# Optimization experiments

Hardware: AMD Instinct MI355X
Metric: run time of the kernel (lower is better)

## Reference

```python
import jax, jax.numpy as jnp
import numpy as np

B, N, M, U, L = 2048, 256, 128, 512, 2   # batch, memory locations, memory width, num_units, num_layers
RH, WH, SH = 2, 2, 1                      # read heads, write heads, conv_shift_range
CLIP = 20.0
HEAD_R = M + 3 + (2 * SH + 1)             # 134 = k(M)+beta+g+s(2r+1)+gamma
HEAD_W = HEAD_R + 2 * M                   # 390 = + erase(M) + add(M)


def setup_inputs():
    key = jax.random.key(0)
    ks = jax.random.split(key, 12)
    def nrm(k, shape, s=0.05):
        return jax.random.normal(k, shape, jnp.float32) * s
    return {
        "X": jax.random.normal(ks[0], (B, U), jnp.float32),
        "m0": nrm(ks[1], (1, N, M), 0.5),
        "H0": nrm(ks[2], (L, 1, U)),
        "C0": nrm(ks[3], (L, 1, U)),
        "R0": nrm(ks[4], (RH, 1, M)),
        "A0": nrm(ks[5], (RH + WH, 1, N)),
        "W_prep": nrm(ks[6], (M * RH, U)),
        "b_prep": jnp.zeros((U,), jnp.float32),
        "W_lstm": nrm(ks[7], (L, 3 * U, 4 * U)),
        "b_lstm": jnp.zeros((L, 4 * U), jnp.float32),
        "W_r": nrm(ks[8], (U, RH * HEAD_R)),
        "b_r": jnp.zeros((RH * HEAD_R,), jnp.float32),
        "W_w": nrm(ks[9], (U, WH * HEAD_W)),
        "b_w": jnp.zeros((WH * HEAD_W,), jnp.float32),
        "W_ou": nrm(ks[10], (U + RH * M, U)),
        "b_ou": jnp.zeros((U,), jnp.float32),
    }


def _addressing(k, beta, g, s, gamma, m, a_prev):
    # k [B,M], beta/g/gamma [B], s [B,2*SH+1], m [B,N,M], a_prev [B,N]
    inner = jnp.einsum('bnm,bm->bn', m, k)
    k_norm = jnp.sqrt(jnp.sum(k * k, axis=1, keepdims=True))   # [B,1]
    m_norm = jnp.sqrt(jnp.sum(m * m, axis=2))                  # [B,N]
    K = inner / (k_norm * m_norm + 1e-8)
    w_c = jax.nn.softmax(beta[:, None] * K, axis=1)            # exp/sum in source == softmax
    w_g = g[:, None] * w_c + (1.0 - g[:, None]) * a_prev
    # The stacked-slice s_matrix in the source is exactly circular convolution:
    # w_conv[i] = sum_d s_d * w_g[(i - d) mod N], d in {0..SH, -SH..-1} matching s layout.
    shifts = list(range(0, SH + 1)) + list(range(-SH, 0))
    w_conv = sum(s[:, j:j + 1] * jnp.roll(w_g, shifts[j], axis=1) for j in range(2 * SH + 1))
    w_sharp = w_conv ** gamma[:, None]
    return w_sharp / jnp.sum(w_sharp, axis=1, keepdims=True)


def reference(X, m0, H0, C0, R0, A0, W_prep, b_prep, W_lstm, b_lstm,
              W_r, b_r, W_w, b_w, W_ou, b_ou):
    b = X.shape[0]
    m = jnp.broadcast_to(m0, (b, N, M))
    R_prev = [jnp.broadcast_to(jnp.tanh(R0[i]), (b, M)) for i in range(RH)]
    A_prev = [jnp.broadcast_to(jax.nn.softmax(A0[i], axis=-1), (b, N)) for i in range(RH + WH)]

    # controller
    h = jnp.concatenate(R_prev, axis=1) @ W_prep + b_prep
    for l in range(L):
        x_in = jnp.concatenate([X, h], axis=1)                              # [B,2U]
        h_prev = jnp.broadcast_to(H0[l], (b, U))
        c_prev = jnp.broadcast_to(C0[l], (b, U))
        z = jnp.concatenate([x_in, h_prev], axis=1) @ W_lstm[l] + b_lstm[l]  # [B,4U]
        i_g, f_g, g_g, o_g = jnp.split(z, 4, axis=1)
        c = jax.nn.sigmoid(f_g) * c_prev + jax.nn.sigmoid(i_g) * jnp.tanh(g_g)
        h = jax.nn.sigmoid(o_g) * jnp.tanh(c)
    h = jnp.clip(h, -CLIP, CLIP)

    r_heads = (h @ W_r + b_r).reshape(b, RH, HEAD_R)
    w_heads = (h @ W_w + b_w).reshape(b, WH, HEAD_W)
    heads = [r_heads[:, i] for i in range(RH)] + [w_heads[:, i] for i in range(WH)]

    A_t = []
    for ii, hd in enumerate(heads):
        A_t.append(_addressing(
            k=jnp.tanh(hd[:, :M]),
            beta=jax.nn.softplus(hd[:, M]),
            g=jax.nn.sigmoid(hd[:, M + 1]),
            s=jax.nn.softmax(hd[:, M + 2:M + 2 + 2 * SH + 1], axis=-1),
            gamma=jax.nn.softplus(hd[:, M + 2 + 2 * SH + 1]),
            m=m, a_prev=A_prev[ii]))

    # reads from old memory
    R_t = [jnp.einsum('bn,bnm->bm', A_t[i], m) for i in range(RH)]

    # sequential erase/add writes
    m_t = m
    for ii in range(WH):
        w = A_t[RH + ii][:, :, None]                                  # [B,N,1]
        del_v = jax.nn.sigmoid(w_heads[:, ii, -2 * M:-M])[:, None, :]  # [B,1,M]
        add_v = jnp.tanh(w_heads[:, ii, -M:])[:, None, :]
        m_t = m_t * (1.0 - w * del_v) + w * add_v

    y = jnp.clip(jnp.concatenate([h] + R_t, axis=1) @ W_ou + b_ou, -CLIP, CLIP)
    return y, m_t
```

## Files before the change

### kernel.cpp

```cpp
#include <hip/hip_runtime.h>
#include <math.h>

static constexpr int Bn = 2048;
static constexpr int Nn = 256;
static constexpr int Mn = 128;
static constexpr int Un = 512;

static constexpr size_t OFF_MNORM = 4608;
static constexpr size_t OFF_APREV = 4864;
static constexpr size_t OFF_BIASH = 5888;
static constexpr size_t OFF_KMAT  = 16384;
static constexpr size_t OFF_HEADS = OFF_KMAT + (size_t)8192 * 256;
static constexpr size_t OFF_AT    = OFF_HEADS + (size_t)2048 * 1048;
static constexpr size_t OFF_ERA   = OFF_AT + (size_t)2 * 2048 * 256;
static constexpr size_t OFF_ADD   = OFF_ERA + (size_t)2048 * 256;
static constexpr size_t OFF_XHB   = OFF_ADD + (size_t)2048 * 256;
static constexpr size_t OFF_HCAT  = OFF_XHB + 524288;
static constexpr size_t OFF_W0T   = OFF_HCAT + 524288;
static constexpr size_t OFF_W1T   = OFF_W0T + 524288;
static constexpr size_t OFF_WRWT  = OFF_W1T + 1048576;
static constexpr size_t OFF_WCOMB = OFF_WRWT + 294912;
static constexpr size_t OFF_WR2T  = OFF_WCOMB + 262144;
static constexpr size_t OFF_M0B   = OFF_WR2T + 65536;
static constexpr size_t OFF_ZPART = OFF_M0B + 16384 + 524288;

static constexpr int S_X0  = 0;
static constexpr int S_M0  = 512;
static constexpr int S_W0  = 528;
static constexpr int S_W1  = 1552;
static constexpr int S_WR  = 3600;
static constexpr int S_WW  = 3744;
static constexpr int S_WOU = 4144;
static constexpr int S_WR2 = 4400;
static constexpr int S_CA  = 4528;
static constexpr int S_ZC  = 4529;
static constexpr int S_END = 4657;

#define DEV __device__ __forceinline__

typedef __attribute__((ext_vector_type(8))) short bf16x8;
typedef __attribute__((ext_vector_type(4))) float f32x4;
typedef __attribute__((ext_vector_type(8))) unsigned short ushort8;
typedef unsigned int u32;

DEV float sigf(float x) { return 1.0f / (1.0f + expf(-x)); }
DEV float softplusf(float x) { return x > 20.0f ? x : log1pf(expf(x)); }
DEV unsigned short f2bf(float f) {
    unsigned u = __float_as_uint(f);
    u = (u + 0x7FFFu + ((u >> 16) & 1u)) >> 16;
    return (unsigned short)u;
}
DEV void gload16(const unsigned short* g, unsigned short* l) {
    __builtin_amdgcn_global_load_lds(
        (const __attribute__((address_space(1))) u32*)g,
        (__attribute__((address_space(3))) u32*)l, 16, 0, 0);
}

DEV float blk_reduce_max(float v, float* red) {
    int tid = threadIdx.x;
    red[tid] = v; __syncthreads();
    for (int s = (int)blockDim.x >> 1; s > 0; s >>= 1) {
        if (tid < s) red[tid] = fmaxf(red[tid], red[tid + s]);
        __syncthreads();
    }
    float r = red[0]; __syncthreads();
    return r;
}
DEV float blk_reduce_sum(float v, float* red) {
    int tid = threadIdx.x;
    red[tid] = v; __syncthreads();
    for (int s = (int)blockDim.x >> 1; s > 0; s >>= 1) {
        if (tid < s) red[tid] += red[tid + s];
        __syncthreads();
    }
    float r = red[0]; __syncthreads();
    return r;
}

DEV float wv_sum(float v) {
    #pragma unroll
    for (int off = 32; off; off >>= 1) v += __shfl_xor(v, off);
    return v;
}
DEV float wv_max(float v) {
    #pragma unroll
    for (int off = 32; off; off >>= 1) v = fmaxf(v, __shfl_xor(v, off));
    return v;
}
DEV float blk_sum4(float v, float* red4) {
    v = wv_sum(v);
    int w = threadIdx.x >> 6;
    if ((threadIdx.x & 63) == 0) red4[w] = v;
    __syncthreads();
    float r = red4[0] + red4[1] + red4[2] + red4[3];
    __syncthreads();
    return r;
}
DEV float blk_max4(float v, float* red4) {
    v = wv_max(v);
    int w = threadIdx.x >> 6;
    if ((threadIdx.x & 63) == 0) red4[w] = v;
    __syncthreads();
    float r = fmaxf(fmaxf(red4[0], red4[1]), fmaxf(red4[2], red4[3]));
    __syncthreads();
    return r;
}

#define GEMM_STAGE(buf, k0)                                                     \
    {                                                                           \
        _Pragma("unroll")                                                       \
        for (int q = 0; q < 2; ++q)                                             \
            gload16(A  + (size_t)(row0 + q * 32 + (tid >> 3)) * lda + (k0) + ke,\
                    &As[buf][q * 2048 + tid * 8]);                              \
        _Pragma("unroll")                                                       \
        for (int q = 0; q < 4; ++q)                                             \
            gload16(Wt + (size_t)(col0 + q * 32 + (tid >> 3)) * ldw + (k0) + ke,\
                    &Ws[buf][q * 2048 + tid * 8]);                              \
    }

#define GEMM_PROLOG_CORE                                                        \
    __shared__ __align__(16) unsigned short As[2][64 * 64];                     \
    __shared__ __align__(16) unsigned short Ws[2][128 * 64];                    \
    const int tid  = threadIdx.x;                                               \
    const int lane = tid & 63;                                                  \
    const int wave = tid >> 6;                                                  \
    const int wr = wave >> 1, wc = wave & 1;                                    \
    const int ke = ((tid & 7) * 8) ^ (((tid >> 3) & 7) << 3);                   \
    const int frow = lane & 15;                                                 \
    const int fko  = (lane >> 4) * 8;                                           \
    const int fxm  = (frow & 7) << 3;                                           \
    f32x4 acc[2][4];                                                            \
    _Pragma("unroll")                                                           \
    for (int i = 0; i < 2; ++i)                                                 \
        _Pragma("unroll")                                                       \
        for (int j = 0; j < 4; ++j) acc[i][j] = (f32x4){0.f, 0.f, 0.f, 0.f};

#define GEMM_PROLOG                                                             \
    GEMM_PROLOG_CORE                                                            \
    const int row0 = blockIdx.x * 64;                                           \
    const int col0 = blockIdx.y * 128;

#define GEMM_FRAGS_AND_MFMA(Ab, Wb)                                             \
    {                                                                           \
        bf16x8 af[2][2], wf[2][4];                                              \
        _Pragma("unroll")                                                       \
        for (int kk = 0; kk < 2; ++kk) {                                        \
            _Pragma("unroll")                                                   \
            for (int i = 0; i < 2; ++i) {                                       \
                int fr = wr * 32 + i * 16 + frow;                               \
                af[kk][i] = *(const bf16x8*)&(Ab)[fr * 64 + ((kk * 32 + fko) ^ fxm)]; \
            }                                                                   \
            _Pragma("unroll")                                                   \
            for (int j = 0; j < 4; ++j) {                                       \
                int fr = wc * 64 + j * 16 + frow;                               \
                wf[kk][j] = *(const bf16x8*)&(Wb)[fr * 64 + ((kk * 32 + fko) ^ fxm)]; \
            }                                                                   \
        }                                                                       \
        __builtin_amdgcn_s_setprio(1);                                          \
        _Pragma("unroll")                                                       \
        for (int kk = 0; kk < 2; ++kk)                                          \
            _Pragma("unroll")                                                   \
            for (int i = 0; i < 2; ++i)                                         \
                _Pragma("unroll")                                               \
                for (int j = 0; j < 4; ++j)                                     \
                    acc[i][j] = __builtin_amdgcn_mfma_f32_16x16x32_bf16(        \
                        af[kk][i], wf[kk][j], acc[i][j], 0, 0, 0);              \
        __builtin_amdgcn_s_setprio(0);                                          \
    }

#define GEMM_MAINLOOP(Kr)                                                       \
    {                                                                           \
        const int nt = (Kr) >> 6;                                               \
        int cur = 0;                                                            \
        GEMM_STAGE(0, 0);                                                       \
        for (int t = 0; t < nt; ++t) {                                          \
            if (t + 1 < nt) {                                                   \
                GEMM_STAGE(cur ^ 1, (t + 1) * 64);                              \
                asm volatile("s_waitcnt vmcnt(6)" ::: "memory");                \
            } else {                                                            \
                asm volatile("s_waitcnt vmcnt(0)" ::: "memory");                \
            }                                                                   \
            __builtin_amdgcn_sched_barrier(0);                                  \
            __builtin_amdgcn_s_barrier();                                       \
            __builtin_amdgcn_sched_barrier(0);                                  \
            GEMM_FRAGS_AND_MFMA(As[cur], Ws[cur]);                              \
            __builtin_amdgcn_sched_barrier(0);                                  \
            __builtin_amdgcn_s_barrier();                                       \
            cur ^= 1;                                                           \
        }                                                                       \
    }

__global__ __launch_bounds__(256) void gemm_bf16(
    const unsigned short* __restrict__ A, int lda,
    const unsigned short* __restrict__ Wt, int ldw,
    const float* __restrict__ bias,
    float* __restrict__ C, unsigned short* __restrict__ Cb, int ldc,
    int Nr, int Kr, int epi)
{
    GEMM_PROLOG
    GEMM_MAINLOOP(Kr)
    #pragma unroll
    for (int i = 0; i < 2; ++i) {
        int m0r = row0 + wr * 32 + i * 16 + (lane >> 4) * 4;
        #pragma unroll
        for (int j = 0; j < 4; ++j) {
            int n = col0 + wc * 64 + j * 16 + (lane & 15);
            if (n >= Nr) continue;
            float bv = bias ? bias[n] : 0.f;
            #pragma unroll
            for (int r = 0; r < 4; ++r) {
                float v = acc[i][j][r] + bv;
                if (epi == 1) v = fminf(fmaxf(v, -20.f), 20.f);
                if (epi == 2) Cb[(size_t)(m0r + r) * ldc + n] = f2bf(v);
                else          C [(size_t)(m0r + r) * ldc + n] = v;
            }
        }
    }
}

__global__ __launch_bounds__(256) void gemm_lstm(
    const unsigned short* __restrict__ A, int lda,
    const unsigned short* __restrict__ Wt, int ldw,
    const float* __restrict__ zpart, const float* __restrict__ b_lstm,
    int z, const float* __restrict__ c0,
    unsigned short* __restrict__ hout, int ldh, int Kr, int doclip)
{
    GEMM_PROLOG
    GEMM_MAINLOOP(Kr)
    const int uu = lane & 15;
    const int q  = (col0 >> 6) + wc;
    const int uq = q * 16 + uu;
    const float c0v = c0[uq];
    float bg[4];
    #pragma unroll
    for (int g = 0; g < 4; ++g) {
        int j = g * 512 + q * 16 + uu;
        float a = b_lstm[z * 2048 + j];
        #pragma unroll
        for (int p = 0; p < 8; ++p)
            a += zpart[((size_t)z * 8 + p) * 2048 + j];
        bg[g] = a;
    }
    #pragma unroll
    for (int i = 0; i < 2; ++i) {
        int rbase = row0 + wr * 32 + i * 16 + (lane >> 4) * 4;
        #pragma unroll
        for (int r = 0; r < 4; ++r) {
            float ig = acc[i][0][r] + bg[0];
            float fg = acc[i][1][r] + bg[1];
            float gg = acc[i][2][r] + bg[2];
            float og = acc[i][3][r] + bg[3];
            float c = sigf(fg) * c0v + sigf(ig) * tanhf(gg);
            float h = sigf(og) * tanhf(c);
            if (doclip) h = fminf(fmaxf(h, -20.f), 20.f);
            hout[(size_t)(rbase + r) * ldh + uq] = f2bf(h);
        }
    }
}

__global__ __launch_bounds__(256) void gemm_l0p(
    const unsigned short* __restrict__ XHB,
    const unsigned short* __restrict__ W0T,
    const unsigned short* __restrict__ WR2T,
    const unsigned short* __restrict__ M0B,
    const float* __restrict__ zpart, const float* __restrict__ b_lstm,
    const float* __restrict__ c0, unsigned short* __restrict__ hout,
    unsigned short* __restrict__ WCOMB)
{
    const int by = blockIdx.y, bx = blockIdx.x;
    const unsigned short *A, *Wt;
    int lda, ldw, row0, col0, Kr;
    unsigned short* pCb = nullptr;
    if (by < 16) {
        A = XHB;  lda = 1024; Wt = W0T; ldw = 512;
        row0 = bx * 64; col0 = by * 128; Kr = 512;
    } else {
        int pz = bx >> 4, py = (bx >> 3) & 1, px = bx & 7;
        A = WR2T + pz * 128; lda = 256; Wt = M0B; ldw = 128;
        row0 = px * 64; col0 = py * 128; Kr = 128;
        pCb = WCOMB + 512 + pz * 256;
    }
    GEMM_PROLOG_CORE
    GEMM_MAINLOOP(Kr)
    if (by < 16) {
        const int uu = lane & 15;
        const int q  = (col0 >> 6) + wc;
        const int uq = q * 16 + uu;
        const float c0v = c0[uq];
        float bg[4];
        #pragma unroll
        for (int g = 0; g < 4; ++g) {
            int j = g * 512 + q * 16 + uu;
            float a = b_lstm[j];
            #pragma unroll
            for (int p = 0; p < 8; ++p)
                a += zpart[(size_t)p * 2048 + j];
            bg[g] = a;
        }
        #pragma unroll
        for (int i = 0; i < 2; ++i) {
            int rbase = row0 + wr * 32 + i * 16 + (lane >> 4) * 4;
            #pragma unroll
            for (int r = 0; r < 4; ++r) {
                float ig = acc[i][0][r] + bg[0];
                float fg = acc[i][1][r] + bg[1];
                float gg = acc[i][2][r] + bg[2];
                float og = acc[i][3][r] + bg[3];
                float c = sigf(fg) * c0v + sigf(ig) * tanhf(gg);
                float h = sigf(og) * tanhf(c);
                hout[(size_t)(rbase + r) * 1024 + uq] = f2bf(h);
            }
        }
    } else {
        #pragma unroll
        for (int i = 0; i < 2; ++i) {
            int m0r = row0 + wr * 32 + i * 16 + (lane >> 4) * 4;
            #pragma unroll
            for (int j = 0; j < 4; ++j) {
                int n = col0 + wc * 64 + j * 16 + (lane & 15);
                #pragma unroll
                for (int r = 0; r < 4; ++r)
                    pCb[(size_t)(m0r + r) * 1024 + n] = f2bf(acc[i][j][r]);
            }
        }
    }
}

__global__ __launch_bounds__(256) void gemm_kmat(
    const float* __restrict__ heads,
    const unsigned short* __restrict__ M0B,
    float* __restrict__ C)
{
    GEMM_PROLOG_CORE
    const int row0 = blockIdx.x * 64;
    const int col0 = blockIdx.y * 128;

#define KMAT_STAGE(buf, k0)                                                     \
    {                                                                           \
        _Pragma("unroll")                                                       \
        for (int q = 0; q < 2; ++q) {                                           \
            int R = row0 + q * 32 + (tid >> 3);                                 \
            int b = R >> 2, ih = R & 3;                                         \
            int cb = (ih < 2) ? ih * 134 : 268 + (ih - 2) * 390;                \
            const float* hp = heads + (size_t)b * 1048 + cb + (k0) + ke;        \
            ushort8 o;                                                          \
            _Pragma("unroll")                                                   \
            for (int j = 0; j < 8; ++j) o[j] = f2bf(tanhf(hp[j]));              \
            *(ushort8*)&As[buf][q * 2048 + tid * 8] = o;                        \
        }                                                                       \
        _Pragma("unroll")                                                       \
        for (int q = 0; q < 4; ++q)                                             \
            gload16(M0B + (size_t)(col0 + q * 32 + (tid >> 3)) * 128 + (k0) + ke,\
                    &Ws[buf][q * 2048 + tid * 8]);                              \
    }

    int cur = 0;
    KMAT_STAGE(0, 0);
    for (int t = 0; t < 2; ++t) {
        __syncthreads();
        if (t == 0) KMAT_STAGE(1, 64);
        GEMM_FRAGS_AND_MFMA(As[cur], Ws[cur]);
        cur ^= 1;
    }
#undef KMAT_STAGE
    #pragma unroll
    for (int i = 0; i < 2; ++i) {
        int m0r = row0 + wr * 32 + i * 16 + (lane >> 4) * 4;
        #pragma unroll
        for (int j = 0; j < 4; ++j) {
            int n = col0 + wc * 64 + j * 16 + (lane & 15);
            #pragma unroll
            for (int r = 0; r < 4; ++r)
                C[(size_t)(m0r + r) * 256 + n] = acc[i][j][r];
        }
    }
}

DEV void dev_cvt8(const float* src, int lds, unsigned short* dst, int ldd,
                  int c8, int bloc, int tid)
{
    size_t idx = (size_t)bloc * 256 + tid;
    size_t r = idx / c8, c = (idx % c8) * 8;
    const float* s = src + r * lds + c;
    float4 v0 = *(const float4*)s;
    float4 v1 = *(const float4*)(s + 4);
    ushort8 o;
    o[0] = f2bf(v0.x); o[1] = f2bf(v0.y); o[2] = f2bf(v0.z); o[3] = f2bf(v0.w);
    o[4] = f2bf(v1.x); o[5] = f2bf(v1.y); o[6] = f2bf(v1.z); o[7] = f2bf(v1.w);
    *(ushort8*)(dst + r * ldd + c) = o;
}

DEV void dev_cvtT(const float* src, int R, int C, int lds,
                  unsigned short* dst, int ldd, int mode, int bx, int by,
                  int tid, float* t )
{
    const int x = tid & 31;
    for (int y = tid >> 5; y < 32; y += 8) {
        int r = by * 32 + y, c = bx * 32 + x;
        int scol = c;
        if (mode) scol = ((c >> 4) & 3) * 512 + (c >> 6) * 16 + (c & 15);
        t[y * 33 + x] = (r < R && c < C) ? src[(size_t)r * lds + scol] : 0.f;
    }
    __syncthreads();
    for (int y = tid >> 5; y < 32; y += 8) {
        int c = bx * 32 + y, r = by * 32 + x;
        if (c < C && r < R) dst[(size_t)c * ldd + r] = f2bf(t[x * 33 + y]);
    }
}

__global__ __launch_bounds__(256) void k_prep(
    const float* __restrict__ X, const float* __restrict__ m0,
    const float* __restrict__ H0, const float* __restrict__ R0,
    const float* __restrict__ A0, const float* __restrict__ W_prep,
    const float* __restrict__ b_prep, const float* __restrict__ W_lstm,
    const float* __restrict__ W_r, const float* __restrict__ b_r,
    const float* __restrict__ W_w, const float* __restrict__ b_w,
    const float* __restrict__ W_ou, float* __restrict__ ws)
{
    __shared__ float sh[32 * 33 + 64];
    const int bid = blockIdx.x, tid = threadIdx.x;
    unsigned short* XHB   = (unsigned short*)(ws + OFF_XHB);
    unsigned short* W0T   = (unsigned short*)(ws + OFF_W0T);
    unsigned short* W1T   = (unsigned short*)(ws + OFF_W1T);
    unsigned short* WRWT  = (unsigned short*)(ws + OFF_WRWT);
    unsigned short* WCOMB = (unsigned short*)(ws + OFF_WCOMB);
    unsigned short* WR2T  = (unsigned short*)(ws + OFF_WR2T);
    unsigned short* M0B   = (unsigned short*)(ws + OFF_M0B);

    if (bid < S_M0) {
        dev_cvt8(X, 512, XHB, 1024, 64, bid - S_X0, tid);
    } else if (bid < S_W0) {
        dev_cvt8(m0, 128, M0B, 128, 16, bid - S_M0, tid);
    } else if (bid < S_W1) {
        int s = bid - S_W0;
        dev_cvtT(W_lstm, 512, 2048, 2048, W0T, 512, 1, s & 63, s >> 6, tid, sh);
    } else if (bid < S_WR) {
        int s = bid - S_W1;
        dev_cvtT(W_lstm + (size_t)1536 * 2048, 1024, 2048, 2048, W1T, 1024, 1,
                 s & 63, s >> 6, tid, sh);
    } else if (bid < S_WW) {
        int s = bid - S_WR;
        dev_cvtT(W_r, 512, 268, 268, WRWT, 512, 0, s % 9, s / 9, tid, sh);
    } else if (bid < S_WOU) {
        int s = bid - S_WW;
        dev_cvtT(W_w, 512, 780, 780, WRWT + (size_t)268 * 512, 512, 0,
                 s % 25, s / 25, tid, sh);
    } else if (bid < S_WR2) {
        int s = bid - S_WOU;
        dev_cvtT(W_ou, 512, 512, 512, WCOMB, 1024, 0, s & 15, s >> 4, tid, sh);
    } else if (bid < S_CA) {
        int s = bid - S_WR2;
        dev_cvtT(W_ou + (size_t)512 * 512, 256, 512, 512, WR2T, 256, 0,
                 s & 15, s >> 4, tid, sh);
    } else if (bid < S_ZC) {
        float* red = sh;
        for (int i = 0; i < 4; ++i) {
            float v = A0[i * 256 + tid];
            float mx = blk_reduce_max(v, red);
            float e = expf(v - mx);
            float s = blk_reduce_sum(e, red);
            ws[OFF_APREV + i * 256 + tid] = e / s;
        }
        float acc = 0.f;
        for (int m = 0; m < 128; ++m) {
            float t = m0[(size_t)tid * 128 + m];
            acc = fmaf(t, t, acc);
        }
        ws[OFF_MNORM + tid] = sqrtf(acc);
        for (int j = tid; j < 1152; j += 256)
            ws[OFF_BIASH + j] = (j < 268) ? b_r[j] : (j < 1048 ? b_w[j - 268] : 0.f);
    } else {
        int sub = bid - S_ZC;
        int colb = sub & 7, up = (sub >> 3) & 7, z = sub >> 6;
        int j = colb * 256 + tid;
        float acc = 0.f;
        if (z == 0) {
            if (up < 4) {
                sh[256 + tid] = tanhf(R0[tid]);
                __syncthreads();
                if (tid < 128) {
                    int u = up * 128 + tid;
                    float a = b_prep[u];
                    for (int k = 0; k < 256; ++k)
                        a = fmaf(sh[256 + k], W_prep[(size_t)k * 512 + u], a);
                    sh[tid] = a;
                }
                __syncthreads();
                const int u0 = up * 128;
                #pragma unroll 4
                for (int t = 0; t < 128; ++t)
                    acc = fmaf(sh[t], W_lstm[(size_t)(512 + u0 + t) * 2048 + j], acc);
            } else {
                const int u0 = up * 128;
                #pragma unroll 4
                for (int t = 0; t < 128; ++t)
                    acc = fmaf(H0[u0 - 512 + t],
                               W_lstm[(size_t)(512 + u0 + t) * 2048 + j], acc);
            }
        } else {
            const int u0 = up * 64;
            const float* W1 = W_lstm + (size_t)1536 * 2048;
            #pragma unroll 4
            for (int t = 0; t < 64; ++t)
                acc = fmaf(H0[512 + u0 + t], W1[(size_t)(1024 + u0 + t) * 2048 + j], acc);
        }
        (ws + OFF_ZPART)[((size_t)z * 8 + up) * 2048 + j] = acc;
    }
}

__global__ __launch_bounds__(256) void k_addr(
    const float* __restrict__ heads, const float* __restrict__ kmat,
    const float* __restrict__ mnorm, const float* __restrict__ aprev,
    float* __restrict__ at, unsigned short* __restrict__ hcat,
    float* __restrict__ era, float* __restrict__ addv)
{
    __shared__ float red4[4];
    __shared__ float wgs[256];
    __shared__ float sc[6];
    const int b = blockIdx.x, i = blockIdx.y, tid = threadIdx.x;
    const int cb = (i < 2) ? i * 134 : 268 + (i - 2) * 390;
    const float* hd = heads + (size_t)b * 1048 + cb;
    float kv = (tid < 128) ? tanhf(hd[tid]) : 0.f;
    float kn = sqrtf(blk_sum4(kv * kv, red4));
    if (i >= 2 && tid < 128) {
        era [((size_t)b * 2 + (i - 2)) * 128 + tid] = sigf(hd[134 + tid]);
        addv[((size_t)b * 2 + (i - 2)) * 128 + tid] = tanhf(hd[262 + tid]);
    }
    if (tid == 0) {
        sc[0] = softplusf(hd[128]);
        sc[1] = sigf(hd[129]);
        float v0 = hd[130], v1 = hd[131], v2 = hd[132];
        float mx = fmaxf(v0, fmaxf(v1, v2));
        float e0 = expf(v0 - mx), e1 = expf(v1 - mx), e2 = expf(v2 - mx);
        float ssum = e0 + e1 + e2;
        sc[2] = e0 / ssum; sc[3] = e1 / ssum; sc[4] = e2 / ssum;
        sc[5] = softplusf(hd[133]);
    }
    __syncthreads();
    const float beta = sc[0], g = sc[1], s0 = sc[2], s1 = sc[3], s2 = sc[4],
                gamma = sc[5];
    float inner = kmat[((size_t)b * 4 + i) * 256 + tid];
    float K = inner / (kn * mnorm[tid] + 1e-8f);
    float x = beta * K;
    float mx = blk_max4(x, red4);
    float e = expf(x - mx);
    float se = blk_sum4(e, red4);
    float wc = e / se;
    float wg = g * wc + (1.f - g) * aprev[i * 256 + tid];
    wgs[tid] = wg;
    __syncthreads();
    float wconv = s0 * wg + s1 * wgs[(tid + 255) & 255] + s2 * wgs[(tid + 1) & 255];
    float wsh = powf(wconv, gamma);
    float ssum = blk_sum4(wsh, red4);
    float w = wsh / ssum;
    if (i < 2) hcat[(size_t)b * 1024 + 512 + i * 256 + tid] = f2bf(w);
    else       at[((size_t)(i - 2) * Bn + b) * 256 + tid] = w;
}

__global__ __launch_bounds__(512) void k_memt(
    const float* __restrict__ m0, const float* __restrict__ at,
    const float* __restrict__ era, const float* __restrict__ addv,
    float* __restrict__ outm)
{
    __shared__ __align__(16) float at_s[2][8][256];
    __shared__ __align__(16) float er_s[2][8][128];
    __shared__ __align__(16) float ad_s[2][8][128];
    const int tid = threadIdx.x;
    const int b0 = blockIdx.x * 8;
    for (int t = tid; t < 1024; t += 512) {
        int i = t >> 9, rem = t & 511;
        int bb = rem >> 6, n4 = rem & 63;
        ((float4*)&at_s[i][bb][0])[n4] =
            ((const float4*)(at + ((size_t)i * Bn + b0 + bb) * 256))[n4];
    }
    {
        int t = tid;
        if (t < 512) {
            int i = t >> 8, rem = t & 255;
            int bb = rem >> 5, m4 = rem & 31;
            ((float4*)&er_s[i][bb][0])[m4] =
                ((const float4*)(era + ((size_t)(b0 + bb) * 2 + i) * 128))[m4];
            ((float4*)&ad_s[i][bb][0])[m4] =
                ((const float4*)(addv + ((size_t)(b0 + bb) * 2 + i) * 128))[m4];
        }
    }
    __syncthreads();
    const float4* m0v = (const float4*)m0;
    float4* outv = (float4*)outm;
    for (int pos = tid; pos < 8192; pos += 512) {
        int mq = pos & 31, n = pos >> 5;
        float4 t0 = m0v[pos];
        #pragma unroll
        for (int bb = 0; bb < 8; ++bb) {
            float w0 = at_s[0][bb][n], w1 = at_s[1][bb][n];
            float4 e0 = *(const float4*)&er_s[0][bb][mq * 4];
            float4 a0 = *(const float4*)&ad_s[0][bb][mq * 4];
            float4 e1 = *(const float4*)&er_s[1][bb][mq * 4];
            float4 a1 = *(const float4*)&ad_s[1][bb][mq * 4];
            float4 t = t0;
#define UPD(c) { t.c = t.c * (1.f - w0 * e0.c) + w0 * a0.c; \
                 t.c = t.c * (1.f - w1 * e1.c) + w1 * a1.c; }
            UPD(x) UPD(y) UPD(z) UPD(w)
#undef UPD
            __builtin_nontemporal_store(*(f32x4*)&t,
                (f32x4*)&outv[(size_t)(b0 + bb) * 8192 + pos]);
        }
    }
}

extern "C" void kernel_launch(void* const* d_in, const int* in_sizes, int n_in,
                              void* d_out, int out_size, void* d_ws, size_t ws_size,
                              hipStream_t stream)
{
    const float* X      = (const float*)d_in[0];
    const float* m0     = (const float*)d_in[1];
    const float* H0     = (const float*)d_in[2];
    const float* C0     = (const float*)d_in[3];
    const float* R0     = (const float*)d_in[4];
    const float* A0     = (const float*)d_in[5];
    const float* W_prep = (const float*)d_in[6];
    const float* b_prep = (const float*)d_in[7];
    const float* W_lstm = (const float*)d_in[8];
    const float* b_lstm = (const float*)d_in[9];
    const float* W_r    = (const float*)d_in[10];
    const float* b_r    = (const float*)d_in[11];
    const float* W_w    = (const float*)d_in[12];
    const float* b_w    = (const float*)d_in[13];
    const float* W_ou   = (const float*)d_in[14];
    const float* b_ou   = (const float*)d_in[15];
    float* ws  = (float*)d_ws;
    float* out = (float*)d_out;

    unsigned short* XHB   = (unsigned short*)(ws + OFF_XHB);
    unsigned short* HCAT  = (unsigned short*)(ws + OFF_HCAT);
    unsigned short* W0T   = (unsigned short*)(ws + OFF_W0T);
    unsigned short* W1T   = (unsigned short*)(ws + OFF_W1T);
    unsigned short* WRWT  = (unsigned short*)(ws + OFF_WRWT);
    unsigned short* WCOMB = (unsigned short*)(ws + OFF_WCOMB);
    unsigned short* WR2T  = (unsigned short*)(ws + OFF_WR2T);
    unsigned short* M0B   = (unsigned short*)(ws + OFF_M0B);

    k_prep<<<S_END, 256, 0, stream>>>(
        X, m0, H0, R0, A0, W_prep, b_prep, W_lstm, W_r, b_r, W_w, b_w, W_ou, ws);

    gemm_l0p<<<dim3(32, 17), 256, 0, stream>>>(
        XHB, W0T, WR2T, M0B, ws + OFF_ZPART, b_lstm, C0, XHB + 512, WCOMB);

    gemm_lstm<<<dim3(32, 16), 256, 0, stream>>>(
        XHB, 1024, W1T, 1024, ws + OFF_ZPART, b_lstm, 1, C0 + 512, HCAT, 1024, 1024, 1);

    gemm_bf16<<<dim3(32, 9), 256, 0, stream>>>(
        HCAT, 1024, WRWT, 512, ws + OFF_BIASH, ws + OFF_HEADS, nullptr, 1048, 1048, 512, 0);

    gemm_kmat<<<dim3(128, 2), 256, 0, stream>>>(
        ws + OFF_HEADS, M0B, ws + OFF_KMAT);

    k_addr<<<dim3(Bn, 4), 256, 0, stream>>>(
        ws + OFF_HEADS, ws + OFF_KMAT, ws + OFF_MNORM, ws + OFF_APREV,
        ws + OFF_AT, HCAT, ws + OFF_ERA, ws + OFF_ADD);

    gemm_bf16<<<dim3(32, 4), 256, 0, stream>>>(
        HCAT, 1024, WCOMB, 1024, b_ou, out, nullptr, 512, 512, 1024, 1);

    k_memt<<<256, 512, 0, stream>>>(
        m0, ws + OFF_AT, ws + OFF_ERA, ws + OFF_ADD, out + (size_t)Bn * Un);
}
```

Measured before the change: 185.3 us.

## Re-partition weight prep across kernels and merge output GEMM with memory write

```diff
diff --git a/kernel.cpp b/kernel.cpp
--- a/kernel.cpp
+++ b/kernel.cpp
@@ -24,17 +24,26 @@
 static constexpr size_t OFF_M0B   = OFF_WR2T + 65536;
 static constexpr size_t OFF_ZPART = OFF_M0B + 16384 + 524288;
 
-static constexpr int S_X0  = 0;
-static constexpr int S_M0  = 512;
-static constexpr int S_W0  = 528;
-static constexpr int S_W1  = 1552;
-static constexpr int S_WR  = 3600;
-static constexpr int S_WW  = 3744;
-static constexpr int S_WOU = 4144;
-static constexpr int S_WR2 = 4400;
-static constexpr int S_CA  = 4528;
-static constexpr int S_ZC  = 4529;
-static constexpr int S_END = 4657;
+static constexpr int P_X0  = 0;
+static constexpr int P_M0  = 512;
+static constexpr int P_W0  = 528;
+static constexpr int P_WR2 = 1552;
+static constexpr int P_CA  = 1680;
+static constexpr int P_ZC  = 1681;
+static constexpr int P_END = 1745;
+
+static constexpr int M_L0  = 0;
+static constexpr int M_PF  = 512;
+static constexpr int M_W1  = 544;
+static constexpr int M_WRr = 2592;
+static constexpr int M_WRw = 2736;
+static constexpr int M_WOU = 3136;
+static constexpr int M_ZC1 = 3392;
+static constexpr int M_END = 3456;
+
+static constexpr int T_OUT = 0;
+static constexpr int T_MEM = 128;
+static constexpr int T_END = 384;
 
 #define DEV __device__ __forceinline__
 
@@ -106,21 +115,11 @@
     return r;
 }
 
-#define GEMM_STAGE(buf, k0)                                                     \
-    {                                                                           \
-        _Pragma("unroll")                                                       \
-        for (int q = 0; q < 2; ++q)                                             \
-            gload16(A  + (size_t)(row0 + q * 32 + (tid >> 3)) * lda + (k0) + ke,\
-                    &As[buf][q * 2048 + tid * 8]);                              \
-        _Pragma("unroll")                                                       \
-        for (int q = 0; q < 4; ++q)                                             \
-            gload16(Wt + (size_t)(col0 + q * 32 + (tid >> 3)) * ldw + (k0) + ke,\
-                    &Ws[buf][q * 2048 + tid * 8]);                              \
-    }
-
-#define GEMM_PROLOG_CORE                                                        \
+#define GEMM_SHARED                                                             \
     __shared__ __align__(16) unsigned short As[2][64 * 64];                     \
-    __shared__ __align__(16) unsigned short Ws[2][128 * 64];                    \
+    __shared__ __align__(16) unsigned short Ws[2][128 * 64];
+
+#define GEMM_REGS                                                               \
     const int tid  = threadIdx.x;                                               \
     const int lane = tid & 63;                                                  \
     const int wave = tid >> 6;                                                  \
@@ -135,10 +134,17 @@
         _Pragma("unroll")                                                       \
         for (int j = 0; j < 4; ++j) acc[i][j] = (f32x4){0.f, 0.f, 0.f, 0.f};
 
-#define GEMM_PROLOG                                                             \
-    GEMM_PROLOG_CORE                                                            \
-    const int row0 = blockIdx.x * 64;                                           \
-    const int col0 = blockIdx.y * 128;
+#define GEMM_STAGE(buf, k0)                                                     \
+    {                                                                           \
+        _Pragma("unroll")                                                       \
+        for (int q = 0; q < 2; ++q)                                             \
+            gload16(A  + (size_t)(row0 + q * 32 + (tid >> 3)) * lda + (k0) + ke,\
+                    &As[buf][q * 2048 + tid * 8]);                              \
+        _Pragma("unroll")                                                       \
+        for (int q = 0; q < 4; ++q)                                             \
+            gload16(Wt + (size_t)(col0 + q * 32 + (tid >> 3)) * ldw + (k0) + ke,\
+                    &Ws[buf][q * 2048 + tid * 8]);                              \
+    }
 
 #define GEMM_FRAGS_AND_MFMA(Ab, Wb)                                             \
     {                                                                           \
@@ -190,14 +196,249 @@
         }                                                                       \
     }
 
+#define LSTM_EPILOGUE(zc, doclip, houtp, ldhv)                                  \
+    {                                                                           \
+        const int uu = lane & 15;                                               \
+        const int q  = (col0 >> 6) + wc;                                        \
+        const int uq = q * 16 + uu;                                             \
+        const float c0v = c0[(zc) * 512 + uq];                                  \
+        float bg[4];                                                            \
+        _Pragma("unroll")                                                       \
+        for (int g = 0; g < 4; ++g) {                                           \
+            int j = g * 512 + q * 16 + uu;                                      \
+            float a = b_lstm[(zc) * 2048 + j];                                  \
+            _Pragma("unroll")                                                   \
+            for (int p = 0; p < 8; ++p)                                         \
+                a += zpart[((size_t)(zc) * 8 + p) * 2048 + j];                  \
+            bg[g] = a;                                                          \
+        }                                                                       \
+        _Pragma("unroll")                                                       \
+        for (int i = 0; i < 2; ++i) {                                           \
+            int rbase = row0 + wr * 32 + i * 16 + (lane >> 4) * 4;              \
+            _Pragma("unroll")                                                   \
+            for (int r = 0; r < 4; ++r) {                                       \
+                float ig = acc[i][0][r] + bg[0];                                \
+                float fg = acc[i][1][r] + bg[1];                                \
+                float gg = acc[i][2][r] + bg[2];                                \
+                float og = acc[i][3][r] + bg[3];                                \
+                float c = sigf(fg) * c0v + sigf(ig) * tanhf(gg);                \
+                float h = sigf(og) * tanhf(c);                                  \
+                if (doclip) h = fminf(fmaxf(h, -20.f), 20.f);                   \
+                (houtp)[(size_t)(rbase + r) * (ldhv) + uq] = f2bf(h);           \
+            }                                                                   \
+        }                                                                       \
+    }
+
+DEV void dev_cvt8(const float* src, int lds, unsigned short* dst, int ldd,
+                  int c8, int bloc, int tid)
+{
+    size_t idx = (size_t)bloc * 256 + tid;
+    size_t r = idx / c8, c = (idx % c8) * 8;
+    const float* s = src + r * lds + c;
+    float4 v0 = *(const float4*)s;
+    float4 v1 = *(const float4*)(s + 4);
+    ushort8 o;
+    o[0] = f2bf(v0.x); o[1] = f2bf(v0.y); o[2] = f2bf(v0.z); o[3] = f2bf(v0.w);
+    o[4] = f2bf(v1.x); o[5] = f2bf(v1.y); o[6] = f2bf(v1.z); o[7] = f2bf(v1.w);
+    *(ushort8*)(dst + r * ldd + c) = o;
+}
+
+DEV void dev_cvtT(const float* src, int R, int C, int lds,
+                  unsigned short* dst, int ldd, int mode, int bx, int by,
+                  int tid, float* t )
+{
+    const int x = tid & 31;
+    for (int y = tid >> 5; y < 32; y += 8) {
+        int r = by * 32 + y, c = bx * 32 + x;
+        int scol = c;
+        if (mode) scol = ((c >> 4) & 3) * 512 + (c >> 6) * 16 + (c & 15);
+        t[y * 33 + x] = (r < R && c < C) ? src[(size_t)r * lds + scol] : 0.f;
+    }
+    __syncthreads();
+    for (int y = tid >> 5; y < 32; y += 8) {
+        int c = bx * 32 + y, r = by * 32 + x;
+        if (c < C && r < R) dst[(size_t)c * ldd + r] = f2bf(t[x * 33 + y]);
+    }
+}
+
+__global__ __launch_bounds__(256) void k_prep(
+    const float* __restrict__ X, const float* __restrict__ m0,
+    const float* __restrict__ H0, const float* __restrict__ R0,
+    const float* __restrict__ A0, const float* __restrict__ W_prep,
+    const float* __restrict__ b_prep, const float* __restrict__ W_lstm,
+    const float* __restrict__ b_r, const float* __restrict__ b_w,
+    const float* __restrict__ W_ou, float* __restrict__ ws)
+{
+    __shared__ float sh[32 * 33 + 64];
+    const int bid = blockIdx.x, tid = threadIdx.x;
+    unsigned short* XHB  = (unsigned short*)(ws + OFF_XHB);
+    unsigned short* W0T  = (unsigned short*)(ws + OFF_W0T);
+    unsigned short* WR2T = (unsigned short*)(ws + OFF_WR2T);
+    unsigned short* M0B  = (unsigned short*)(ws + OFF_M0B);
+
+    if (bid < P_M0) {
+        dev_cvt8(X, 512, XHB, 1024, 64, bid - P_X0, tid);
+    } else if (bid < P_W0) {
+        dev_cvt8(m0, 128, M0B, 128, 16, bid - P_M0, tid);
+    } else if (bid < P_WR2) {
+        int s = bid - P_W0;
+        dev_cvtT(W_lstm, 512, 2048, 2048, W0T, 512, 1, s & 63, s >> 6, tid, sh);
+    } else if (bid < P_CA) {
+        int s = bid - P_WR2;
+        dev_cvtT(W_ou + (size_t)512 * 512, 256, 512, 512, WR2T, 256, 0,
+                 s & 15, s >> 4, tid, sh);
+    } else if (bid < P_ZC) {
+        float* red = sh;
+        for (int i = 0; i < 4; ++i) {
+            float v = A0[i * 256 + tid];
+            float mx = blk_reduce_max(v, red);
+            float e = expf(v - mx);
+            float s = blk_reduce_sum(e, red);
+            ws[OFF_APREV + i * 256 + tid] = e / s;
+        }
+        float acc = 0.f;
+        for (int m = 0; m < 128; ++m) {
+            float t = m0[(size_t)tid * 128 + m];
+            acc = fmaf(t, t, acc);
+        }
+        ws[OFF_MNORM + tid] = sqrtf(acc);
+        for (int j = tid; j < 1152; j += 256)
+            ws[OFF_BIASH + j] = (j < 268) ? b_r[j] : (j < 1048 ? b_w[j - 268] : 0.f);
+    } else {
+        int sub = bid - P_ZC;
+        int colb = sub & 7, up = sub >> 3;
+        int j = colb * 256 + tid;
+        float acc = 0.f;
+        if (up < 4) {
+            sh[256 + tid] = tanhf(R0[tid]);
+            __syncthreads();
+            if (tid < 128) {
+                int u = up * 128 + tid;
+                float a = b_prep[u];
+                for (int k = 0; k < 256; ++k)
+                    a = fmaf(sh[256 + k], W_prep[(size_t)k * 512 + u], a);
+                sh[tid] = a;
+            }
+            __syncthreads();
+            const int u0 = up * 128;
+            #pragma unroll 4
+            for (int t = 0; t < 128; ++t)
+                acc = fmaf(sh[t], W_lstm[(size_t)(512 + u0 + t) * 2048 + j], acc);
+        } else {
+            const int u0 = up * 128;
+            #pragma unroll 4
+            for (int t = 0; t < 128; ++t)
+                acc = fmaf(H0[u0 - 512 + t],
+                           W_lstm[(size_t)(512 + u0 + t) * 2048 + j], acc);
+        }
+        (ws + OFF_ZPART)[(size_t)up * 2048 + j] = acc;
+    }
+}
+
+__global__ __launch_bounds__(256) void k_mid(
+    const float* __restrict__ W_lstm, const float* __restrict__ W_r,
+    const float* __restrict__ W_w, const float* __restrict__ W_ou,
+    const float* __restrict__ H0, const float* __restrict__ b_lstm,
+    const float* __restrict__ c0, float* __restrict__ ws)
+{
+    GEMM_SHARED
+    const int s = blockIdx.x;
+    float* sh = (float*)&As[0][0];
+    unsigned short* XHB   = (unsigned short*)(ws + OFF_XHB);
+    unsigned short* W0T   = (unsigned short*)(ws + OFF_W0T);
+    unsigned short* W1T   = (unsigned short*)(ws + OFF_W1T);
+    unsigned short* WRWT  = (unsigned short*)(ws + OFF_WRWT);
+    unsigned short* WCOMB = (unsigned short*)(ws + OFF_WCOMB);
+    unsigned short* WR2T  = (unsigned short*)(ws + OFF_WR2T);
+    unsigned short* M0B   = (unsigned short*)(ws + OFF_M0B);
+    const float* zpart    = ws + OFF_ZPART;
+
+    if (s < M_W1) {
+        const unsigned short *A, *Wt;
+        int lda, ldw, row0, col0, Kr;
+        unsigned short* pCb = nullptr;
+        const bool lstm0 = (s < M_PF);
+        if (lstm0) {
+            A = XHB;  lda = 1024; Wt = W0T; ldw = 512;
+            row0 = (s & 31) * 64; col0 = (s >> 5) * 128; Kr = 512;
+        } else {
+            int p = s - M_PF;
+            int pz = p >> 4, py = (p >> 3) & 1, px = p & 7;
+            A = WR2T + pz * 128; lda = 256; Wt = M0B; ldw = 128;
+            row0 = px * 64; col0 = py * 128; Kr = 128;
+            pCb = WCOMB + 512 + pz * 256;
+        }
+        GEMM_REGS
+        GEMM_MAINLOOP(Kr)
+        if (lstm0) {
+            unsigned short* hout = XHB + 512;
+            LSTM_EPILOGUE(0, 0, hout, 1024)
+        } else {
+            #pragma unroll
+            for (int i = 0; i < 2; ++i) {
+                int m0r = row0 + wr * 32 + i * 16 + (lane >> 4) * 4;
+                #pragma unroll
+                for (int j = 0; j < 4; ++j) {
+                    int n = col0 + wc * 64 + j * 16 + (lane & 15);
+                    #pragma unroll
+                    for (int r = 0; r < 4; ++r)
+                        pCb[(size_t)(m0r + r) * 1024 + n] = f2bf(acc[i][j][r]);
+                }
+            }
+        }
+    } else if (s < M_WRr) {
+        int s1 = s - M_W1;
+        dev_cvtT(W_lstm + (size_t)1536 * 2048, 1024, 2048, 2048, W1T, 1024, 1,
+                 s1 & 63, s1 >> 6, threadIdx.x, sh);
+    } else if (s < M_WRw) {
+        int s2 = s - M_WRr;
+        dev_cvtT(W_r, 512, 268, 268, WRWT, 512, 0, s2 % 9, s2 / 9, threadIdx.x, sh);
+    } else if (s < M_WOU) {
+        int s3 = s - M_WRw;
+        dev_cvtT(W_w, 512, 780, 780, WRWT + (size_t)268 * 512, 512, 0,
+                 s3 % 25, s3 / 25, threadIdx.x, sh);
+    } else if (s < M_ZC1) {
+        int s4 = s - M_WOU;
+        dev_cvtT(W_ou, 512, 512, 512, WCOMB, 1024, 0, s4 & 15, s4 >> 4,
+                 threadIdx.x, sh);
+    } else {
+        int s5 = s - M_ZC1;
+        int colb = s5 & 7, up = s5 >> 3;
+        int j = colb * 256 + threadIdx.x;
+        const int u0 = up * 64;
+        const float* W1 = W_lstm + (size_t)1536 * 2048;
+        float acc = 0.f;
+        #pragma unroll 4
+        for (int t = 0; t < 64; ++t)
+            acc = fmaf(H0[512 + u0 + t], W1[(size_t)(1024 + u0 + t) * 2048 + j], acc);
+        (ws + OFF_ZPART)[((size_t)8 + up) * 2048 + j] = acc;
+    }
+}
+
+__global__ __launch_bounds__(256) void gemm_lstm(
+    const unsigned short* __restrict__ A, int lda,
+    const unsigned short* __restrict__ Wt, int ldw,
+    const float* __restrict__ zpart, const float* __restrict__ b_lstm,
+    const float* __restrict__ c0, unsigned short* __restrict__ hout)
+{
+    GEMM_SHARED
+    const int row0 = blockIdx.x * 64;
+    const int col0 = blockIdx.y * 128;
+    GEMM_REGS
+    GEMM_MAINLOOP(1024)
+    LSTM_EPILOGUE(1, 1, hout, 1024)
+}
+
 __global__ __launch_bounds__(256) void gemm_bf16(
     const unsigned short* __restrict__ A, int lda,
     const unsigned short* __restrict__ Wt, int ldw,
-    const float* __restrict__ bias,
-    float* __restrict__ C, unsigned short* __restrict__ Cb, int ldc,
-    int Nr, int Kr, int epi)
-{
-    GEMM_PROLOG
+    const float* __restrict__ bias, float* __restrict__ C, int ldc,
+    int Nr, int Kr)
+{
+    GEMM_SHARED
+    const int row0 = blockIdx.x * 64;
+    const int col0 = blockIdx.y * 128;
+    GEMM_REGS
     GEMM_MAINLOOP(Kr)
     #pragma unroll
     for (int i = 0; i < 2; ++i) {
@@ -208,120 +449,8 @@
             if (n >= Nr) continue;
             float bv = bias ? bias[n] : 0.f;
             #pragma unroll
-            for (int r = 0; r < 4; ++r) {
-                float v = acc[i][j][r] + bv;
-                if (epi == 1) v = fminf(fmaxf(v, -20.f), 20.f);
-                if (epi == 2) Cb[(size_t)(m0r + r) * ldc + n] = f2bf(v);
-                else          C [(size_t)(m0r + r) * ldc + n] = v;
-            }
-        }
-    }
-}
-
-__global__ __launch_bounds__(256) void gemm_lstm(
-    const unsigned short* __restrict__ A, int lda,
-    const unsigned short* __restrict__ Wt, int ldw,
-    const float* __restrict__ zpart, const float* __restrict__ b_lstm,
-    int z, const float* __restrict__ c0,
-    unsigned short* __restrict__ hout, int ldh, int Kr, int doclip)
-{
-    GEMM_PROLOG
-    GEMM_MAINLOOP(Kr)
-    const int uu = lane & 15;
-    const int q  = (col0 >> 6) + wc;
-    const int uq = q * 16 + uu;
-    const float c0v = c0[uq];
-    float bg[4];
-    #pragma unroll
-    for (int g = 0; g < 4; ++g) {
-        int j = g * 512 + q * 16 + uu;
-        float a = b_lstm[z * 2048 + j];
-        #pragma unroll
-        for (int p = 0; p < 8; ++p)
-            a += zpart[((size_t)z * 8 + p) * 2048 + j];
-        bg[g] = a;
-    }
-    #pragma unroll
-    for (int i = 0; i < 2; ++i) {
-        int rbase = row0 + wr * 32 + i * 16 + (lane >> 4) * 4;
-        #pragma unroll
-        for (int r = 0; r < 4; ++r) {
-            float ig = acc[i][0][r] + bg[0];
-            float fg = acc[i][1][r] + bg[1];
-            float gg = acc[i][2][r] + bg[2];
-            float og = acc[i][3][r] + bg[3];
-            float c = sigf(fg) * c0v + sigf(ig) * tanhf(gg);
-            float h = sigf(og) * tanhf(c);
-            if (doclip) h = fminf(fmaxf(h, -20.f), 20.f);
-            hout[(size_t)(rbase + r) * ldh + uq] = f2bf(h);
-        }
-    }
-}
-
-__global__ __launch_bounds__(256) void gemm_l0p(
-    const unsigned short* __restrict__ XHB,
-    const unsigned short* __restrict__ W0T,
-    const unsigned short* __restrict__ WR2T,
-    const unsigned short* __restrict__ M0B,
-    const float* __restrict__ zpart, const float* __restrict__ b_lstm,
-    const float* __restrict__ c0, unsigned short* __restrict__ hout,
-    unsigned short* __restrict__ WCOMB)
-{
-    const int by = blockIdx.y, bx = blockIdx.x;
-    const unsigned short *A, *Wt;
-    int lda, ldw, row0, col0, Kr;
-    unsigned short* pCb = nullptr;
-    if (by < 16) {
-        A = XHB;  lda = 1024; Wt = W0T; ldw = 512;
-        row0 = bx * 64; col0 = by * 128; Kr = 512;
-    } else {
-        int pz = bx >> 4, py = (bx >> 3) & 1, px = bx & 7;
-        A = WR2T + pz * 128; lda = 256; Wt = M0B; ldw = 128;
-        row0 = px * 64; col0 = py * 128; Kr = 128;
-        pCb = WCOMB + 512 + pz * 256;
-    }
-    GEMM_PROLOG_CORE
-    GEMM_MAINLOOP(Kr)
-    if (by < 16) {
-        const int uu = lane & 15;
-        const int q  = (col0 >> 6) + wc;
-        const int uq = q * 16 + uu;
-        const float c0v = c0[uq];
-        float bg[4];
-        #pragma unroll
-        for (int g = 0; g < 4; ++g) {
-            int j = g * 512 + q * 16 + uu;
-            float a = b_lstm[j];
-            #pragma unroll
-            for (int p = 0; p < 8; ++p)
-                a += zpart[(size_t)p * 2048 + j];
-            bg[g] = a;
-        }
-        #pragma unroll
-        for (int i = 0; i < 2; ++i) {
-            int rbase = row0 + wr * 32 + i * 16 + (lane >> 4) * 4;
-            #pragma unroll
-            for (int r = 0; r < 4; ++r) {
-                float ig = acc[i][0][r] + bg[0];
-                float fg = acc[i][1][r] + bg[1];
-                float gg = acc[i][2][r] + bg[2];
-                float og = acc[i][3][r] + bg[3];
-                float c = sigf(fg) * c0v + sigf(ig) * tanhf(gg);
-                float h = sigf(og) * tanhf(c);
-                hout[(size_t)(rbase + r) * 1024 + uq] = f2bf(h);
-            }
-        }
-    } else {
-        #pragma unroll
-        for (int i = 0; i < 2; ++i) {
-            int m0r = row0 + wr * 32 + i * 16 + (lane >> 4) * 4;
-            #pragma unroll
-            for (int j = 0; j < 4; ++j) {
-                int n = col0 + wc * 64 + j * 16 + (lane & 15);
-                #pragma unroll
-                for (int r = 0; r < 4; ++r)
-                    pCb[(size_t)(m0r + r) * 1024 + n] = f2bf(acc[i][j][r]);
-            }
+            for (int r = 0; r < 4; ++r)
+                C[(size_t)(m0r + r) * ldc + n] = acc[i][j][r] + bv;
         }
     }
 }
@@ -331,9 +460,10 @@
     const unsigned short* __restrict__ M0B,
     float* __restrict__ C)
 {
-    GEMM_PROLOG_CORE
+    GEMM_SHARED
     const int row0 = blockIdx.x * 64;
     const int col0 = blockIdx.y * 128;
+    GEMM_REGS
 
 #define KMAT_STAGE(buf, k0)                                                     \
     {                                                                           \
@@ -373,138 +503,6 @@
             for (int r = 0; r < 4; ++r)
                 C[(size_t)(m0r + r) * 256 + n] = acc[i][j][r];
         }
-    }
-}
-
-DEV void dev_cvt8(const float* src, int lds, unsigned short* dst, int ldd,
-                  int c8, int bloc, int tid)
-{
-    size_t idx = (size_t)bloc * 256 + tid;
-    size_t r = idx / c8, c = (idx % c8) * 8;
-    const float* s = src + r * lds + c;
-    float4 v0 = *(const float4*)s;
-    float4 v1 = *(const float4*)(s + 4);
-    ushort8 o;
-    o[0] = f2bf(v0.x); o[1] = f2bf(v0.y); o[2] = f2bf(v0.z); o[3] = f2bf(v0.w);
-    o[4] = f2bf(v1.x); o[5] = f2bf(v1.y); o[6] = f2bf(v1.z); o[7] = f2bf(v1.w);
-    *(ushort8*)(dst + r * ldd + c) = o;
-}
-
-DEV void dev_cvtT(const float* src, int R, int C, int lds,
-                  unsigned short* dst, int ldd, int mode, int bx, int by,
-                  int tid, float* t )
-{
-    const int x = tid & 31;
-    for (int y = tid >> 5; y < 32; y += 8) {
-        int r = by * 32 + y, c = bx * 32 + x;
-        int scol = c;
-        if (mode) scol = ((c >> 4) & 3) * 512 + (c >> 6) * 16 + (c & 15);
-        t[y * 33 + x] = (r < R && c < C) ? src[(size_t)r * lds + scol] : 0.f;
-    }
-    __syncthreads();
-    for (int y = tid >> 5; y < 32; y += 8) {
-        int c = bx * 32 + y, r = by * 32 + x;
-        if (c < C && r < R) dst[(size_t)c * ldd + r] = f2bf(t[x * 33 + y]);
-    }
-}
-
-__global__ __launch_bounds__(256) void k_prep(
-    const float* __restrict__ X, const float* __restrict__ m0,
-    const float* __restrict__ H0, const float* __restrict__ R0,
-    const float* __restrict__ A0, const float* __restrict__ W_prep,
-    const float* __restrict__ b_prep, const float* __restrict__ W_lstm,
-    const float* __restrict__ W_r, const float* __restrict__ b_r,
-    const float* __restrict__ W_w, const float* __restrict__ b_w,
-    const float* __restrict__ W_ou, float* __restrict__ ws)
-{
-    __shared__ float sh[32 * 33 + 64];
-    const int bid = blockIdx.x, tid = threadIdx.x;
-    unsigned short* XHB   = (unsigned short*)(ws + OFF_XHB);
-    unsigned short* W0T   = (unsigned short*)(ws + OFF_W0T);
-    unsigned short* W1T   = (unsigned short*)(ws + OFF_W1T);
-    unsigned short* WRWT  = (unsigned short*)(ws + OFF_WRWT);
-    unsigned short* WCOMB = (unsigned short*)(ws + OFF_WCOMB);
-    unsigned short* WR2T  = (unsigned short*)(ws + OFF_WR2T);
-    unsigned short* M0B   = (unsigned short*)(ws + OFF_M0B);
-
-    if (bid < S_M0) {
-        dev_cvt8(X, 512, XHB, 1024, 64, bid - S_X0, tid);
-    } else if (bid < S_W0) {
-        dev_cvt8(m0, 128, M0B, 128, 16, bid - S_M0, tid);
-    } else if (bid < S_W1) {
-        int s = bid - S_W0;
-        dev_cvtT(W_lstm, 512, 2048, 2048, W0T, 512, 1, s & 63, s >> 6, tid, sh);
-    } else if (bid < S_WR) {
-        int s = bid - S_W1;
-        dev_cvtT(W_lstm + (size_t)1536 * 2048, 1024, 2048, 2048, W1T, 1024, 1,
-                 s & 63, s >> 6, tid, sh);
-    } else if (bid < S_WW) {
-        int s = bid - S_WR;
-        dev_cvtT(W_r, 512, 268, 268, WRWT, 512, 0, s % 9, s / 9, tid, sh);
-    } else if (bid < S_WOU) {
-        int s = bid - S_WW;
-        dev_cvtT(W_w, 512, 780, 780, WRWT + (size_t)268 * 512, 512, 0,
-                 s % 25, s / 25, tid, sh);
-    } else if (bid < S_WR2) {
-        int s = bid - S_WOU;
-        dev_cvtT(W_ou, 512, 512, 512, WCOMB, 1024, 0, s & 15, s >> 4, tid, sh);
-    } else if (bid < S_CA) {
-        int s = bid - S_WR2;
-        dev_cvtT(W_ou + (size_t)512 * 512, 256, 512, 512, WR2T, 256, 0,
-                 s & 15, s >> 4, tid, sh);
-    } else if (bid < S_ZC) {
-        float* red = sh;
-        for (int i = 0; i < 4; ++i) {
-            float v = A0[i * 256 + tid];
-            float mx = blk_reduce_max(v, red);
-            float e = expf(v - mx);
-            float s = blk_reduce_sum(e, red);
-            ws[OFF_APREV + i * 256 + tid] = e / s;
-        }
-        float acc = 0.f;
-        for (int m = 0; m < 128; ++m) {
-            float t = m0[(size_t)tid * 128 + m];
-            acc = fmaf(t, t, acc);
-        }
-        ws[OFF_MNORM + tid] = sqrtf(acc);
-        for (int j = tid; j < 1152; j += 256)
-            ws[OFF_BIASH + j] = (j < 268) ? b_r[j] : (j < 1048 ? b_w[j - 268] : 0.f);
-    } else {
-        int sub = bid - S_ZC;
-        int colb = sub & 7, up = (sub >> 3) & 7, z = sub >> 6;
-        int j = colb * 256 + tid;
-        float acc = 0.f;
-        if (z == 0) {
-            if (up < 4) {
-                sh[256 + tid] = tanhf(R0[tid]);
-                __syncthreads();
-                if (tid < 128) {
-                    int u = up * 128 + tid;
-                    float a = b_prep[u];
-                    for (int k = 0; k < 256; ++k)
-                        a = fmaf(sh[256 + k], W_prep[(size_t)k * 512 + u], a);
-                    sh[tid] = a;
-                }
-                __syncthreads();
-                const int u0 = up * 128;
-                #pragma unroll 4
-                for (int t = 0; t < 128; ++t)
-                    acc = fmaf(sh[t], W_lstm[(size_t)(512 + u0 + t) * 2048 + j], acc);
-            } else {
-                const int u0 = up * 128;
-                #pragma unroll 4
-                for (int t = 0; t < 128; ++t)
-                    acc = fmaf(H0[u0 - 512 + t],
-                               W_lstm[(size_t)(512 + u0 + t) * 2048 + j], acc);
-            }
-        } else {
-            const int u0 = up * 64;
-            const float* W1 = W_lstm + (size_t)1536 * 2048;
-            #pragma unroll 4
-            for (int t = 0; t < 64; ++t)
-                acc = fmaf(H0[512 + u0 + t], W1[(size_t)(1024 + u0 + t) * 2048 + j], acc);
-        }
-        (ws + OFF_ZPART)[((size_t)z * 8 + up) * 2048 + j] = acc;
     }
 }
 
@@ -557,25 +555,51 @@
     else       at[((size_t)(i - 2) * Bn + b) * 256 + tid] = w;
 }
 
-__global__ __launch_bounds__(512) void k_memt(
+__global__ __launch_bounds__(256) void k_tail(
+    const unsigned short* __restrict__ HCAT,
+    const unsigned short* __restrict__ WCOMB,
+    const float* __restrict__ b_ou,
     const float* __restrict__ m0, const float* __restrict__ at,
     const float* __restrict__ era, const float* __restrict__ addv,
-    float* __restrict__ outm)
-{
-    __shared__ __align__(16) float at_s[2][8][256];
-    __shared__ __align__(16) float er_s[2][8][128];
-    __shared__ __align__(16) float ad_s[2][8][128];
-    const int tid = threadIdx.x;
-    const int b0 = blockIdx.x * 8;
-    for (int t = tid; t < 1024; t += 512) {
-        int i = t >> 9, rem = t & 511;
-        int bb = rem >> 6, n4 = rem & 63;
-        ((float4*)&at_s[i][bb][0])[n4] =
-            ((const float4*)(at + ((size_t)i * Bn + b0 + bb) * 256))[n4];
-    }
-    {
-        int t = tid;
-        if (t < 512) {
+    float* __restrict__ out)
+{
+    GEMM_SHARED
+    const int s = blockIdx.x;
+    if (s < T_MEM) {
+        const unsigned short* A  = HCAT;  const int lda = 1024;
+        const unsigned short* Wt = WCOMB; const int ldw = 1024;
+        const int row0 = (s & 31) * 64;
+        const int col0 = (s >> 5) * 128;
+        GEMM_REGS
+        GEMM_MAINLOOP(1024)
+        #pragma unroll
+        for (int i = 0; i < 2; ++i) {
+            int m0r = row0 + wr * 32 + i * 16 + (lane >> 4) * 4;
+            #pragma unroll
+            for (int j = 0; j < 4; ++j) {
+                int n = col0 + wc * 64 + j * 16 + (lane & 15);
+                if (n >= 512) continue;
+                float bv = b_ou[n];
+                #pragma unroll
+                for (int r = 0; r < 4; ++r) {
+                    float v = acc[i][j][r] + bv;
+                    out[(size_t)(m0r + r) * 512 + n] = fminf(fmaxf(v, -20.f), 20.f);
+                }
+            }
+        }
+    } else {
+        const int tid = threadIdx.x;
+        const int b0 = (s - T_MEM) * 8;
+        float (*at_s)[8][256] = (float(*)[8][256])(&As[0][0]);
+        float (*er_s)[8][128] = (float(*)[8][128])(&Ws[0][0]);
+        float (*ad_s)[8][128] = (float(*)[8][128])(&Ws[0][4096]);
+        for (int t = tid; t < 1024; t += 256) {
+            int i = t >> 9, rem = t & 511;
+            int bb = rem >> 6, n4 = rem & 63;
+            ((float4*)&at_s[i][bb][0])[n4] =
+                ((const float4*)(at + ((size_t)i * Bn + b0 + bb) * 256))[n4];
+        }
+        for (int t = tid; t < 512; t += 256) {
             int i = t >> 8, rem = t & 255;
             int bb = rem >> 5, m4 = rem & 31;
             ((float4*)&er_s[i][bb][0])[m4] =
@@ -583,27 +607,27 @@
             ((float4*)&ad_s[i][bb][0])[m4] =
                 ((const float4*)(addv + ((size_t)(b0 + bb) * 2 + i) * 128))[m4];
         }
-    }
-    __syncthreads();
-    const float4* m0v = (const float4*)m0;
-    float4* outv = (float4*)outm;
-    for (int pos = tid; pos < 8192; pos += 512) {
-        int mq = pos & 31, n = pos >> 5;
-        float4 t0 = m0v[pos];
-        #pragma unroll
-        for (int bb = 0; bb < 8; ++bb) {
-            float w0 = at_s[0][bb][n], w1 = at_s[1][bb][n];
-            float4 e0 = *(const float4*)&er_s[0][bb][mq * 4];
-            float4 a0 = *(const float4*)&ad_s[0][bb][mq * 4];
-            float4 e1 = *(const float4*)&er_s[1][bb][mq * 4];
-            float4 a1 = *(const float4*)&ad_s[1][bb][mq * 4];
-            float4 t = t0;
+        __syncthreads();
+        const float4* m0v = (const float4*)m0;
+        float4* outv = (float4*)(out + (size_t)Bn * Un);
+        for (int pos = tid; pos < 8192; pos += 256) {
+            int mq = pos & 31, n = pos >> 5;
+            float4 t0 = m0v[pos];
+            #pragma unroll
+            for (int bb = 0; bb < 8; ++bb) {
+                float w0 = at_s[0][bb][n], w1 = at_s[1][bb][n];
+                float4 e0 = *(const float4*)&er_s[0][bb][mq * 4];
+                float4 a0 = *(const float4*)&ad_s[0][bb][mq * 4];
+                float4 e1 = *(const float4*)&er_s[1][bb][mq * 4];
+                float4 a1 = *(const float4*)&ad_s[1][bb][mq * 4];
+                float4 t = t0;
 #define UPD(c) { t.c = t.c * (1.f - w0 * e0.c) + w0 * a0.c; \
                  t.c = t.c * (1.f - w1 * e1.c) + w1 * a1.c; }
-            UPD(x) UPD(y) UPD(z) UPD(w)
+                UPD(x) UPD(y) UPD(z) UPD(w)
 #undef UPD
-            __builtin_nontemporal_store(*(f32x4*)&t,
-                (f32x4*)&outv[(size_t)(b0 + bb) * 8192 + pos]);
+                __builtin_nontemporal_store(*(f32x4*)&t,
+                    (f32x4*)&outv[(size_t)(b0 + bb) * 8192 + pos]);
+            }
         }
     }
 }
@@ -633,24 +657,22 @@
 
     unsigned short* XHB   = (unsigned short*)(ws + OFF_XHB);
     unsigned short* HCAT  = (unsigned short*)(ws + OFF_HCAT);
-    unsigned short* W0T   = (unsigned short*)(ws + OFF_W0T);
     unsigned short* W1T   = (unsigned short*)(ws + OFF_W1T);
     unsigned short* WRWT  = (unsigned short*)(ws + OFF_WRWT);
     unsigned short* WCOMB = (unsigned short*)(ws + OFF_WCOMB);
-    unsigned short* WR2T  = (unsigned short*)(ws + OFF_WR2T);
     unsigned short* M0B   = (unsigned short*)(ws + OFF_M0B);
 
-    k_prep<<<S_END, 256, 0, stream>>>(
-        X, m0, H0, R0, A0, W_prep, b_prep, W_lstm, W_r, b_r, W_w, b_w, W_ou, ws);
-
-    gemm_l0p<<<dim3(32, 17), 256, 0, stream>>>(
-        XHB, W0T, WR2T, M0B, ws + OFF_ZPART, b_lstm, C0, XHB + 512, WCOMB);
+    k_prep<<<P_END, 256, 0, stream>>>(
+        X, m0, H0, R0, A0, W_prep, b_prep, W_lstm, b_r, b_w, W_ou, ws);
+
+    k_mid<<<M_END, 256, 0, stream>>>(
+        W_lstm, W_r, W_w, W_ou, H0, b_lstm, C0, ws);
 
     gemm_lstm<<<dim3(32, 16), 256, 0, stream>>>(
-        XHB, 1024, W1T, 1024, ws + OFF_ZPART, b_lstm, 1, C0 + 512, HCAT, 1024, 1024, 1);
+        XHB, 1024, W1T, 1024, ws + OFF_ZPART, b_lstm, C0, HCAT);
 
     gemm_bf16<<<dim3(32, 9), 256, 0, stream>>>(
-        HCAT, 1024, WRWT, 512, ws + OFF_BIASH, ws + OFF_HEADS, nullptr, 1048, 1048, 512, 0);
+        HCAT, 1024, WRWT, 512, ws + OFF_BIASH, ws + OFF_HEADS, 1048, 1048, 512);
 
     gemm_kmat<<<dim3(128, 2), 256, 0, stream>>>(
         ws + OFF_HEADS, M0B, ws + OFF_KMAT);
@@ -659,9 +681,6 @@
         ws + OFF_HEADS, ws + OFF_KMAT, ws + OFF_MNORM, ws + OFF_APREV,
         ws + OFF_AT, HCAT, ws + OFF_ERA, ws + OFF_ADD);
 
-    gemm_bf16<<<dim3(32, 4), 256, 0, stream>>>(
-        HCAT, 1024, WCOMB, 1024, b_ou, out, nullptr, 512, 512, 1024, 1);
-
-    k_memt<<<256, 512, 0, stream>>>(
-        m0, ws + OFF_AT, ws + OFF_ERA, ws + OFF_ADD, out + (size_t)Bn * Un);
-}
+    k_tail<<<T_END, 256, 0, stream>>>(
+        HCAT, WCOMB, b_ou, m0, ws + OFF_AT, ws + OFF_ERA, ws + OFF_ADD, out);
+}
```

After: 175.7 us. -5.2%, faster.
